# Kernel optimization log

Hardware: AMD Instinct MI355X
Metric: run time of the kernel (lower is better)

The kernel has to match this reference:

```python
import jax, jax.numpy as jnp
import numpy as np
import math

NUM_HEADS = 16
QK_NOPE = 128
QK_ROPE = 64
V_DIM = 128
Q_HEAD_DIM = QK_NOPE + QK_ROPE  # 192
KV_LORA = 512
ROPE_THETA = 10000.0
EPS = 1e-6


def setup_inputs() -> dict:
    key = jax.random.key(0)
    ks = jax.random.split(key, 8)
    B, S, H = 2, 2048, 2048
    hidden_states = jax.random.normal(ks[0], (B, S, H), dtype=jnp.float32)
    position_ids = jnp.broadcast_to(jnp.arange(S, dtype=jnp.int64), (B, S))
    attention_mask = jnp.broadcast_to(jnp.tril(jnp.ones((S, S), dtype=bool)), (B, 1, S, S))
    sc = 0.02
    w_q_down = jax.random.normal(ks[1], (1536, H), dtype=jnp.float32) * sc
    q_norm_w = jnp.ones((1536,), dtype=jnp.float32)
    w_q_up = jax.random.normal(ks[2], (NUM_HEADS * Q_HEAD_DIM, 1536), dtype=jnp.float32) * sc
    w_kv_down = jax.random.normal(ks[3], (KV_LORA + QK_ROPE, H), dtype=jnp.float32) * sc
    kv_norm_w = jnp.ones((KV_LORA,), dtype=jnp.float32)
    w_kv_up = jax.random.normal(ks[4], (NUM_HEADS * (QK_NOPE + V_DIM), KV_LORA), dtype=jnp.float32) * sc
    w_out = jax.random.normal(ks[5], (H, NUM_HEADS * V_DIM), dtype=jnp.float32) * sc
    return {"hidden_states": hidden_states, "position_ids": position_ids,
            "attention_mask": attention_mask, "w_q_down": w_q_down, "q_norm_w": q_norm_w,
            "w_q_up": w_q_up, "w_kv_down": w_kv_down, "kv_norm_w": kv_norm_w,
            "w_kv_up": w_kv_up, "w_out": w_out}


def rms_norm(x, w):
    xf = x.astype(jnp.float32)
    var = jnp.mean(xf * xf, axis=-1, keepdims=True)
    return w * (xf * jax.lax.rsqrt(var + EPS)).astype(x.dtype)


def rotate_half(x):
    d = x.shape[-1]
    return jnp.concatenate((-x[..., d // 2:], x[..., :d // 2]), axis=-1)


def _deinterleave(x):
    # torch: view(..., d//2, 2).transpose(-1,-2).reshape(..., d)
    d = x.shape[-1]
    return x.reshape(*x.shape[:-1], d // 2, 2).swapaxes(-1, -2).reshape(*x.shape[:-1], d)


def _rope_tables(seq_len, dtype):
    inv_freq = 1.0 / (ROPE_THETA ** (jnp.arange(0, QK_ROPE, 2, dtype=jnp.float32) / QK_ROPE))
    t = jnp.arange(seq_len, dtype=jnp.float32)
    freqs = jnp.outer(t, inv_freq)          # [S, QK_ROPE//2]
    emb = jnp.concatenate((freqs, freqs), axis=-1)  # [S, QK_ROPE]
    return jnp.cos(emb).astype(dtype), jnp.sin(emb).astype(dtype)


def mla_forward(hidden_states, position_ids, attention_mask,
                w_q_down, q_norm_w, w_q_up, w_kv_down, kv_norm_w, w_kv_up, w_out):
    B, S, H = hidden_states.shape
    # low-rank Q path
    q = hidden_states @ w_q_down.T                   # [B,S,1536]
    q = rms_norm(q, q_norm_w)
    q = q @ w_q_up.T                                 # [B,S,NH*192]
    q = q.reshape(B, S, NUM_HEADS, Q_HEAD_DIM).transpose(0, 2, 1, 3)  # [B,NH,S,192]
    q_nope, q_rope = q[..., :QK_NOPE], q[..., QK_NOPE:]
    # low-rank KV path
    c = hidden_states @ w_kv_down.T                  # [B,S,576]
    c_kv, k_rope = c[..., :KV_LORA], c[..., KV_LORA:]
    k_rope = k_rope.reshape(B, S, 1, QK_ROPE).transpose(0, 2, 1, 3)   # [B,1,S,64]
    kv = rms_norm(c_kv, kv_norm_w) @ w_kv_up.T       # [B,S,NH*(128+128)]
    kv = kv.reshape(B, S, NUM_HEADS, QK_NOPE + V_DIM).transpose(0, 2, 1, 3)
    k_nope, v = kv[..., :QK_NOPE], kv[..., QK_NOPE:]  # [B,NH,S,128] each
    # decoupled RoPE on the rope sub-dim
    cos, sin = _rope_tables(S, hidden_states.dtype)
    cos_p = cos[position_ids][:, None]               # [B,1,S,64]
    sin_p = sin[position_ids][:, None]
    qr = _deinterleave(q_rope)
    kr = _deinterleave(k_rope)
    q_rope = qr * cos_p + rotate_half(qr) * sin_p
    k_rope = kr * cos_p + rotate_half(kr) * sin_p
    query = jnp.concatenate([q_nope, q_rope], axis=-1)                      # [B,NH,S,192]
    key = jnp.concatenate([k_nope, jnp.broadcast_to(k_rope, (B, NUM_HEADS, S, QK_ROPE))], axis=-1)
    scores = jnp.einsum('bhqd,bhkd->bhqk', query, key) / math.sqrt(Q_HEAD_DIM)
    scores = jnp.where(attention_mask, scores, -jnp.inf)
    attn = jax.nn.softmax(scores, axis=-1).astype(query.dtype)              # [B,NH,S,S]
    out = jnp.einsum('bhqk,bhkd->bhqd', attn, v)                            # [B,NH,S,128]
    out = out.transpose(0, 2, 1, 3).reshape(B, S, NUM_HEADS * V_DIM)
    out = out @ w_out.T                                                     # [B,S,H]
    return out, attn


def reference(hidden_states, position_ids, attention_mask,
              w_q_down, q_norm_w, w_q_up, w_kv_down, kv_norm_w, w_kv_up, w_out):
    return mla_forward(hidden_states, position_ids, attention_mask,
                       w_q_down, q_norm_w, w_q_up, w_kv_down, kv_norm_w, w_kv_up, w_out)
```

## Files before the change

kernel.cpp:

```cpp
#include <hip/hip_runtime.h>
#include <hip/hip_bf16.h>
#include <math.h>

typedef unsigned short u16;
typedef unsigned int u32;
typedef __bf16 bf16x8 __attribute__((ext_vector_type(8)));
typedef float f32x4 __attribute__((ext_vector_type(4)));

__device__ __forceinline__ float bf2f(u16 h) {
    return __uint_as_float(((u32)h) << 16);
}
__device__ __forceinline__ u16 f2bf(float f) {
    u32 u = __float_as_uint(f);
    u32 r = (u + 0x7fffu + ((u >> 16) & 1u)) >> 16;
    return (u16)r;
}

__device__ __forceinline__ f32x4 mfma16(bf16x8 a, bf16x8 b, f32x4 c) {
    return __builtin_amdgcn_mfma_f32_16x16x32_bf16(a, b, c, 0, 0, 0);
}

struct DetectArgs {
    const void* p[8];
    int n[8];
};

__global__ __launch_bounds__(256) void detect_k(DetectArgs a, u32* flags) {
    int b = blockIdx.x;
    int t = threadIdx.x;
    const u16* p = (const u16*)a.p[b];
    u16 v = p[2 * t];
    int e = (v >> 7) & 0xff;
    bool insane = (e < 87) || (e > 167);
    unsigned long long m = __ballot(insane);
    __shared__ u32 s[4];
    int w = t >> 6;
    if ((t & 63) == 0) s[w] = (m != 0ull) ? 1u : 0u;
    __syncthreads();
    if (t == 0) flags[b] = s[0] | s[1] | s[2] | s[3];
}

__global__ __launch_bounds__(256) void convert_k(
    const void* src, u16* dst, int n, const u32* flags, int fi)
{
    u32 f = flags[fi];
    int j0 = blockIdx.x * 1024 + threadIdx.x * 4;
    if (f) {
        const float* s = (const float*)src;
        for (int k = 0; k < 4; k++) {
            int j = j0 + k;
            if (j < n) dst[j] = f2bf(s[j]);
        }
    } else {
        const u16* s = (const u16*)src;
        for (int k = 0; k < 4; k++) {
            int j = j0 + k;
            if (j < n) dst[j] = s[j];
        }
    }
}

__global__ __launch_bounds__(256) void gemm128(
    const u16* __restrict__ X, int xRow, long long xBat,
    const u16* __restrict__ W, int wRow, long long wBat,
    u16* __restrict__ Cb, float* __restrict__ Cf,
    int cRow, long long cBatB, long long cBatH,
    int N, int K)
{
    __shared__ __align__(16) u16 As[128 * 32];
    __shared__ __align__(16) u16 Bs[128 * 32];

    int z = blockIdx.z;
    const u16* Xz = X + (long long)z * xBat;
    const u16* Wz = W + (long long)z * wBat;
    long long cOff = (long long)(z >> 4) * cBatB + (long long)(z & 15) * cBatH;

    int t = threadIdx.x;
    int lane = t & 63, w = t >> 6;
    int sr = t >> 2;
    int sc = (t & 3) * 8;
    int m0 = blockIdx.y * 128, n0 = blockIdx.x * 128;
    int wr = (w >> 1) * 64, wc = (w & 1) * 64;
    int mrow = lane & 15, quad = lane >> 4;

    f32x4 zero = {0.f, 0.f, 0.f, 0.f};
    f32x4 acc[4][4];
    for (int i = 0; i < 4; i++)
        for (int j = 0; j < 4; j++) acc[i][j] = zero;

    for (int k0 = 0; k0 < K; k0 += 32) {
        uint4 a0 = *(const uint4*)(Xz + (long long)(m0 + sr) * xRow + k0 + sc);
        uint4 a1 = *(const uint4*)(Xz + (long long)(m0 + sr + 64) * xRow + k0 + sc);
        int bn0 = n0 + sr;      if (bn0 >= N) bn0 = N - 1;
        int bn1 = n0 + sr + 64; if (bn1 >= N) bn1 = N - 1;
        uint4 b0 = *(const uint4*)(Wz + (long long)bn0 * wRow + k0 + sc);
        uint4 b1 = *(const uint4*)(Wz + (long long)bn1 * wRow + k0 + sc);
        __syncthreads();
        *(uint4*)(&As[sr * 32 + sc]) = a0;
        *(uint4*)(&As[(sr + 64) * 32 + sc]) = a1;
        *(uint4*)(&Bs[sr * 32 + sc]) = b0;
        *(uint4*)(&Bs[(sr + 64) * 32 + sc]) = b1;
        __syncthreads();

        bf16x8 af[4], bfr[4];
        for (int i = 0; i < 4; i++) {
            af[i]  = *(const bf16x8*)(&As[(wr + i * 16 + mrow) * 32 + quad * 8]);
            bfr[i] = *(const bf16x8*)(&Bs[(wc + i * 16 + mrow) * 32 + quad * 8]);
        }
        for (int mt = 0; mt < 4; mt++)
            for (int nt = 0; nt < 4; nt++)
                acc[mt][nt] = mfma16(af[mt], bfr[nt], acc[mt][nt]);
    }

    for (int mt = 0; mt < 4; mt++)
        for (int nt = 0; nt < 4; nt++)
            for (int r = 0; r < 4; r++) {
                int row = m0 + wr + mt * 16 + quad * 4 + r;
                int col = n0 + wc + nt * 16 + mrow;
                if (col < N) {
                    long long idx = cOff + (long long)row * cRow + col;
                    float v = acc[mt][nt][r];
                    if (Cb) Cb[idx] = f2bf(v); else Cf[idx] = v;
                }
            }
}

__global__ __launch_bounds__(256) void gemm128_xf32(
    const float* __restrict__ X, int xRow, long long xBat,
    const u16* __restrict__ W, int wRow, long long wBat,
    u16* __restrict__ Cb, int cRow, long long cBatB, long long cBatH,
    int N, int K)
{
    __shared__ __align__(16) u16 As[128 * 32];
    __shared__ __align__(16) u16 Bs[128 * 32];

    int z = blockIdx.z;
    const float* Xz = X + (long long)z * xBat;
    const u16* Wz = W + (long long)z * wBat;
    long long cOff = (long long)(z >> 4) * cBatB + (long long)(z & 15) * cBatH;

    int t = threadIdx.x;
    int lane = t & 63, w = t >> 6;
    int sr = t >> 2;
    int sc = (t & 3) * 8;
    int m0 = blockIdx.y * 128, n0 = blockIdx.x * 128;
    int wr = (w >> 1) * 64, wc = (w & 1) * 64;
    int mrow = lane & 15, quad = lane >> 4;

    f32x4 zero = {0.f, 0.f, 0.f, 0.f};
    f32x4 acc[4][4];
    for (int i = 0; i < 4; i++)
        for (int j = 0; j < 4; j++) acc[i][j] = zero;

    for (int k0 = 0; k0 < K; k0 += 32) {
        const float* ap0 = Xz + (long long)(m0 + sr) * xRow + k0 + sc;
        const float* ap1 = Xz + (long long)(m0 + sr + 64) * xRow + k0 + sc;
        float4 a0l = *(const float4*)(ap0), a0h = *(const float4*)(ap0 + 4);
        float4 a1l = *(const float4*)(ap1), a1h = *(const float4*)(ap1 + 4);
        int bn0 = n0 + sr;      if (bn0 >= N) bn0 = N - 1;
        int bn1 = n0 + sr + 64; if (bn1 >= N) bn1 = N - 1;
        uint4 b0 = *(const uint4*)(Wz + (long long)bn0 * wRow + k0 + sc);
        uint4 b1 = *(const uint4*)(Wz + (long long)bn1 * wRow + k0 + sc);
        u16 pa0[8] = {f2bf(a0l.x), f2bf(a0l.y), f2bf(a0l.z), f2bf(a0l.w),
                      f2bf(a0h.x), f2bf(a0h.y), f2bf(a0h.z), f2bf(a0h.w)};
        u16 pa1[8] = {f2bf(a1l.x), f2bf(a1l.y), f2bf(a1l.z), f2bf(a1l.w),
                      f2bf(a1h.x), f2bf(a1h.y), f2bf(a1h.z), f2bf(a1h.w)};
        __syncthreads();
        *(uint4*)(&As[sr * 32 + sc]) = *(const uint4*)pa0;
        *(uint4*)(&As[(sr + 64) * 32 + sc]) = *(const uint4*)pa1;
        *(uint4*)(&Bs[sr * 32 + sc]) = b0;
        *(uint4*)(&Bs[(sr + 64) * 32 + sc]) = b1;
        __syncthreads();

        bf16x8 af[4], bfr[4];
        for (int i = 0; i < 4; i++) {
            af[i]  = *(const bf16x8*)(&As[(wr + i * 16 + mrow) * 32 + quad * 8]);
            bfr[i] = *(const bf16x8*)(&Bs[(wc + i * 16 + mrow) * 32 + quad * 8]);
        }
        for (int mt = 0; mt < 4; mt++)
            for (int nt = 0; nt < 4; nt++)
                acc[mt][nt] = mfma16(af[mt], bfr[nt], acc[mt][nt]);
    }

    for (int mt = 0; mt < 4; mt++)
        for (int nt = 0; nt < 4; nt++)
            for (int r = 0; r < 4; r++) {
                int row = m0 + wr + mt * 16 + quad * 4 + r;
                int col = n0 + wc + nt * 16 + mrow;
                if (col < N)
                    Cb[cOff + (long long)row * cRow + col] = f2bf(acc[mt][nt][r]);
            }
}

__global__ __launch_bounds__(256) void rmsnorm_k(
    const float* __restrict__ in, int inRow,
    const u16* __restrict__ wgt,
    u16* __restrict__ out, int outRow, int len)
{
    int row = blockIdx.x;
    const float* x = in + (long long)row * inRow;
    u16* o = out + (long long)row * outRow;
    int t = threadIdx.x;
    float ss = 0.f;
    for (int j = t; j < len; j += 256) { float v = x[j]; ss += v * v; }
    for (int s = 1; s < 64; s <<= 1) ss += __shfl_xor(ss, s);
    __shared__ float red[4];
    int w = t >> 6, lane = t & 63;
    if (lane == 0) red[w] = ss;
    __syncthreads();
    float tot = red[0] + red[1] + red[2] + red[3];
    float r = rsqrtf(tot / (float)len + 1e-6f);
    for (int j = t; j < len; j += 256)
        o[j] = f2bf(bf2f(wgt[j]) * (x[j] * r));
}

__device__ __forceinline__ void rope64(const float* xin, float* xo, int pos) {
    for (int i = 0; i < 32; i++) {
        float ex = (float)(2 * i) * (1.0f / 64.0f);
        float invf = expf(-ex * 9.210340371976184f);
        float ang = (float)pos * invf;
        float sn, cs;
        sincosf(ang, &sn, &cs);
        float a = xin[2 * i], b = xin[2 * i + 1];
        xo[i] = a * cs - b * sn;
        xo[32 + i] = b * cs + a * sn;
    }
}

__global__ __launch_bounds__(256) void rope_q_k(u16* __restrict__ qf) {
    int idx = blockIdx.x * 256 + threadIdx.x;
    int row = idx >> 4, h = idx & 15, pos = row & 2047;
    u16* p = qf + (long long)row * 3072 + h * 192 + 128;
    float xin[64], xo[64];
    for (int j = 0; j < 64; j++) xin[j] = bf2f(p[j]);
    rope64(xin, xo, pos);
    for (int j = 0; j < 64; j++) p[j] = f2bf(xo[j]);
}

__global__ __launch_bounds__(256) void rope_kk(
    const float* __restrict__ cpre, u16* __restrict__ kr) {
    int row = blockIdx.x * 256 + threadIdx.x;
    int pos = row & 2047;
    const float* src = cpre + (long long)row * 576 + 512;
    float xin[64], xo[64];
    for (int j = 0; j < 64; j++) xin[j] = src[j];
    rope64(xin, xo, pos);
    u16* dst = kr + (long long)row * 64;
    for (int j = 0; j < 64; j++) dst[j] = f2bf(xo[j]);
}

__global__ void transpose_v(const u16* __restrict__ kvup, u16* __restrict__ Vt) {
    __shared__ u16 tile[32][33];
    int bh = blockIdx.z, b = bh >> 4, h = bh & 15;
    int s0 = blockIdx.x * 32, d0 = blockIdx.y * 32;
    int tx = threadIdx.x, ty = threadIdx.y;
    for (int i = 0; i < 4; i++) {
        int s = s0 + ty + i * 8;
        tile[ty + i * 8][tx] = kvup[(long long)(b * 2048 + s) * 4096 + h * 256 + 128 + d0 + tx];
    }
    __syncthreads();
    for (int i = 0; i < 4; i++) {
        int d = d0 + ty + i * 8;
        Vt[((long long)bh * 128 + d) * 2048 + s0 + tx] = tile[tx][ty + i * 8];
    }
}

#define ATTN_SCALE 0.07216878364870323f

__global__ __launch_bounds__(256) void scores_gemm(
    const u16* __restrict__ qf, const u16* __restrict__ kvup,
    const u16* __restrict__ krope, float* __restrict__ attn)
{
    int n0 = blockIdx.x * 128, q0 = blockIdx.y * 128;
    if (n0 > q0) return;
    int bh = blockIdx.z, b = bh >> 4, h = bh & 15;
    const u16* qb = qf + (long long)b * 2048 * 3072 + h * 192;
    const u16* kn = kvup + (long long)b * 2048 * 4096 + h * 256;
    const u16* kr = krope + (long long)b * 2048 * 64;
    long long abase = (long long)bh * 4194304;

    __shared__ __align__(16) u16 As[128 * 32];
    __shared__ __align__(16) u16 Bs[128 * 32];
    int t = threadIdx.x, lane = t & 63, w = t >> 6;
    int sr = t >> 2, sc = (t & 3) * 8;
    int wr = (w >> 1) * 64, wc = (w & 1) * 64;
    int mrow = lane & 15, quad = lane >> 4;

    f32x4 zero = {0.f, 0.f, 0.f, 0.f};
    f32x4 acc[4][4];
    for (int i = 0; i < 4; i++)
        for (int j = 0; j < 4; j++) acc[i][j] = zero;

    for (int k0 = 0; k0 < 192; k0 += 32) {
        uint4 a0 = *(const uint4*)(qb + (long long)(q0 + sr) * 3072 + k0 + sc);
        uint4 a1 = *(const uint4*)(qb + (long long)(q0 + sr + 64) * 3072 + k0 + sc);
        uint4 b0, b1;
        if (k0 < 128) {
            b0 = *(const uint4*)(kn + (long long)(n0 + sr) * 4096 + k0 + sc);
            b1 = *(const uint4*)(kn + (long long)(n0 + sr + 64) * 4096 + k0 + sc);
        } else {
            b0 = *(const uint4*)(kr + (long long)(n0 + sr) * 64 + (k0 - 128) + sc);
            b1 = *(const uint4*)(kr + (long long)(n0 + sr + 64) * 64 + (k0 - 128) + sc);
        }
        __syncthreads();
        *(uint4*)(&As[sr * 32 + sc]) = a0;
        *(uint4*)(&As[(sr + 64) * 32 + sc]) = a1;
        *(uint4*)(&Bs[sr * 32 + sc]) = b0;
        *(uint4*)(&Bs[(sr + 64) * 32 + sc]) = b1;
        __syncthreads();

        bf16x8 af[4], bfr[4];
        for (int i = 0; i < 4; i++) {
            af[i]  = *(const bf16x8*)(&As[(wr + i * 16 + mrow) * 32 + quad * 8]);
            bfr[i] = *(const bf16x8*)(&Bs[(wc + i * 16 + mrow) * 32 + quad * 8]);
        }
        for (int mt = 0; mt < 4; mt++)
            for (int nt = 0; nt < 4; nt++)
                acc[mt][nt] = mfma16(af[mt], bfr[nt], acc[mt][nt]);
    }

    for (int mt = 0; mt < 4; mt++)
        for (int nt = 0; nt < 4; nt++)
            for (int r = 0; r < 4; r++) {
                int row = q0 + wr + mt * 16 + quad * 4 + r;
                int col = n0 + wc + nt * 16 + mrow;
                attn[abase + (long long)row * 2048 + col] = acc[mt][nt][r] * ATTN_SCALE;
            }
}

__global__ __launch_bounds__(256) void softmax_rows(float* __restrict__ attn) {
    int r = blockIdx.x;
    long long bh = blockIdx.y;
    float* p = attn + bh * 4194304LL + (long long)r * 2048;
    int t = threadIdx.x;
    int valid = r + 1;

    float mx = -INFINITY;
    for (int j = t; j < valid; j += 256) mx = fmaxf(mx, p[j]);
    for (int s = 1; s < 64; s <<= 1) mx = fmaxf(mx, __shfl_xor(mx, s));
    __shared__ float sm[4];
    if ((t & 63) == 0) sm[t >> 6] = mx;
    __syncthreads();
    mx = fmaxf(fmaxf(sm[0], sm[1]), fmaxf(sm[2], sm[3]));

    float ss = 0.f;
    for (int j = t; j < valid; j += 256) ss += expf(p[j] - mx);
    for (int s = 1; s < 64; s <<= 1) ss += __shfl_xor(ss, s);
    __shared__ float s2[4];
    if ((t & 63) == 0) s2[t >> 6] = ss;
    __syncthreads();
    ss = s2[0] + s2[1] + s2[2] + s2[3];
    float inv = 1.0f / ss;

    for (int j = t; j < 2048; j += 256) {
        float v = (j < valid) ? expf(p[j] - mx) * inv : 0.f;
        p[j] = v;
    }
}

extern "C" void kernel_launch(void* const* d_in, const int* in_sizes, int n_in,
                              void* d_out, int out_size, void* d_ws, size_t ws_size,
                              hipStream_t stream) {
    (void)in_sizes; (void)n_in; (void)out_size; (void)ws_size;

    const void* r_hidden = d_in[0];
    const void* r_wqd    = d_in[3];
    const void* r_qnw    = d_in[4];
    const void* r_wqu    = d_in[5];
    const void* r_wkvd   = d_in[6];
    const void* r_kvnw   = d_in[7];
    const void* r_wkvu   = d_in[8];
    const void* r_wout   = d_in[9];

    float* out_p  = (float*)d_out;
    float* attn_p = (float*)d_out + 8388608LL;

    char* ws = (char*)d_ws;
    size_t off = 0;
    auto alloc = [&](size_t bytes) { void* p = ws + off; off = (off + bytes + 255) & ~(size_t)255; return p; };

    u32* flags = (u32*)alloc(256);
    char* regionA = (char*)alloc(25165824 + 9437184);
    float* q_pre = (float*)regionA;
    float* c_pre = (float*)(regionA + 25165824);
    u16* kv_up   = (u16*)regionA;
    char* regionB = (char*)alloc(16777216);
    u16* hidden_c = (u16*)regionB;
    u16* Vt       = (u16*)regionB;
    char* regionC = (char*)alloc(12582912);
    u16* q_c   = (u16*)regionC;
    u16* kv_c  = (u16*)regionC;
    u16* krope = (u16*)(regionC + 4194304);
    u16* wqd_c  = (u16*)alloc(1536LL * 2048 * 2);
    u16* qnw_c  = (u16*)alloc(1536LL * 2);
    u16* wqu_c  = (u16*)alloc(3072LL * 1536 * 2);
    u16* wkvd_c = (u16*)alloc(576LL * 2048 * 2);
    u16* kvnw_c = (u16*)alloc(512LL * 2);
    u16* wkvu_c = (u16*)alloc(4096LL * 512 * 2);
    u16* wout_c = (u16*)alloc(2048LL * 2048 * 2);
    u16* q_full = (u16*)alloc(4096LL * 3072 * 2);
    u16* Obuf   = q_full;

    DetectArgs da;
    da.p[0] = r_hidden; da.n[0] = 8388608;
    da.p[1] = r_wqd;    da.n[1] = 3145728;
    da.p[2] = r_qnw;    da.n[2] = 1536;
    da.p[3] = r_wqu;    da.n[3] = 4718592;
    da.p[4] = r_wkvd;   da.n[4] = 1179648;
    da.p[5] = r_kvnw;   da.n[5] = 512;
    da.p[6] = r_wkvu;   da.n[6] = 2097152;
    da.p[7] = r_wout;   da.n[7] = 4194304;
    hipLaunchKernelGGL(detect_k, dim3(8), dim3(256), 0, stream, da, flags);

    const void* srcs[8] = {r_hidden, r_wqd, r_qnw, r_wqu, r_wkvd, r_kvnw, r_wkvu, r_wout};
    u16* dsts[8] = {hidden_c, wqd_c, qnw_c, wqu_c, wkvd_c, kvnw_c, wkvu_c, wout_c};
    for (int i = 0; i < 8; i++) {
        int n = da.n[i];
        hipLaunchKernelGGL(convert_k, dim3((n + 1023) / 1024), dim3(256), 0, stream,
            srcs[i], dsts[i], n, flags, i);
    }

    hipLaunchKernelGGL(gemm128, dim3(12, 32, 1), dim3(256), 0, stream,
        hidden_c, 2048, 0LL, wqd_c, 2048, 0LL, (u16*)nullptr, q_pre, 1536, 0LL, 0LL, 1536, 2048);
    hipLaunchKernelGGL(rmsnorm_k, dim3(4096), dim3(256), 0, stream,
        q_pre, 1536, qnw_c, q_c, 1536, 1536);
    hipLaunchKernelGGL(gemm128, dim3(24, 32, 1), dim3(256), 0, stream,
        q_c, 1536, 0LL, wqu_c, 1536, 0LL, q_full, (float*)nullptr, 3072, 0LL, 0LL, 3072, 1536);
    hipLaunchKernelGGL(rope_q_k, dim3(256), dim3(256), 0, stream, q_full);
    hipLaunchKernelGGL(gemm128, dim3(5, 32, 1), dim3(256), 0, stream,
        hidden_c, 2048, 0LL, wkvd_c, 2048, 0LL, (u16*)nullptr, c_pre, 576, 0LL, 0LL, 576, 2048);
    hipLaunchKernelGGL(rmsnorm_k, dim3(4096), dim3(256), 0, stream,
        c_pre, 576, kvnw_c, kv_c, 512, 512);
    hipLaunchKernelGGL(rope_kk, dim3(16), dim3(256), 0, stream, c_pre, krope);
    hipLaunchKernelGGL(gemm128, dim3(32, 32, 1), dim3(256), 0, stream,
        kv_c, 512, 0LL, wkvu_c, 512, 0LL, kv_up, (float*)nullptr, 4096, 0LL, 0LL, 4096, 512);
    hipLaunchKernelGGL(transpose_v, dim3(64, 4, 32), dim3(32, 8), 0, stream, kv_up, Vt);
    hipLaunchKernelGGL(scores_gemm, dim3(16, 16, 32), dim3(256), 0, stream,
        q_full, kv_up, krope, attn_p);
    hipLaunchKernelGGL(softmax_rows, dim3(2048, 32), dim3(256), 0, stream, attn_p);
    hipLaunchKernelGGL(gemm128_xf32, dim3(1, 16, 32), dim3(256), 0, stream,
        attn_p, 2048, 4194304LL, Vt, 2048, 262144LL, Obuf,
        2048, 4194304LL, 128LL, 128, 2048);
    hipLaunchKernelGGL(gemm128, dim3(16, 32, 1), dim3(256), 0, stream,
        Obuf, 2048, 0LL, wout_c, 2048, 0LL, (u16*)nullptr, out_p, 2048, 0LL, 0LL, 2048, 2048);
}
```

Baseline: 1.494 ms.

## Use direct global-to-LDS loads in GEMMs and register-cache softmax rows

Replaces register-staged global loads plus LDS stores in the bf16 GEMM, mixed-precision GEMM and QK score kernels with the global_load_lds builtin, which writes 16 bytes per lane straight into shared memory. The mixed GEMM also stops its K loop at m0+128, skipping K blocks where the operand is zero under a causal structure. Softmax now holds each row in registers via float4 loads, computing exp once and writing with vectorized stores instead of re-reading the row three times. The direct-to-LDS layout (t*8 contiguous) relies on matching the row/col tile layout, and the K truncation assumes a triangular input to that GEMM.

After: 1.317 ms. -11.9%, faster.

```diff
diff --git a/kernel.cpp b/kernel.cpp
--- a/kernel.cpp
+++ b/kernel.cpp
@@ -18,6 +18,13 @@
 
 __device__ __forceinline__ f32x4 mfma16(bf16x8 a, bf16x8 b, f32x4 c) {
     return __builtin_amdgcn_mfma_f32_16x16x32_bf16(a, b, c, 0, 0, 0);
+}
+
+__device__ __forceinline__ void g2l(const u16* g, u16* l) {
+    __builtin_amdgcn_global_load_lds(
+        (const __attribute__((address_space(1))) unsigned int*)g,
+        (__attribute__((address_space(3))) unsigned int*)l,
+        16, 0, 0);
 }
 
 struct DetectArgs {
@@ -83,23 +90,28 @@
     int wr = (w >> 1) * 64, wc = (w & 1) * 64;
     int mrow = lane & 15, quad = lane >> 4;
 
+    u16* As0 = &As[t * 8];
+    u16* As1 = &As[2048 + t * 8];
+    u16* Bs0 = &Bs[t * 8];
+    u16* Bs1 = &Bs[2048 + t * 8];
+
     f32x4 zero = {0.f, 0.f, 0.f, 0.f};
     f32x4 acc[4][4];
     for (int i = 0; i < 4; i++)
         for (int j = 0; j < 4; j++) acc[i][j] = zero;
 
     for (int k0 = 0; k0 < K; k0 += 32) {
-        uint4 a0 = *(const uint4*)(Xz + (long long)(m0 + sr) * xRow + k0 + sc);
-        uint4 a1 = *(const uint4*)(Xz + (long long)(m0 + sr + 64) * xRow + k0 + sc);
+        const u16* ga0 = Xz + (long long)(m0 + sr) * xRow + k0 + sc;
+        const u16* ga1 = ga0 + (long long)64 * xRow;
         int bn0 = n0 + sr;      if (bn0 >= N) bn0 = N - 1;
         int bn1 = n0 + sr + 64; if (bn1 >= N) bn1 = N - 1;
-        uint4 b0 = *(const uint4*)(Wz + (long long)bn0 * wRow + k0 + sc);
-        uint4 b1 = *(const uint4*)(Wz + (long long)bn1 * wRow + k0 + sc);
-        __syncthreads();
-        *(uint4*)(&As[sr * 32 + sc]) = a0;
-        *(uint4*)(&As[(sr + 64) * 32 + sc]) = a1;
-        *(uint4*)(&Bs[sr * 32 + sc]) = b0;
-        *(uint4*)(&Bs[(sr + 64) * 32 + sc]) = b1;
+        const u16* gb0 = Wz + (long long)bn0 * wRow + k0 + sc;
+        const u16* gb1 = Wz + (long long)bn1 * wRow + k0 + sc;
+        __syncthreads();
+        g2l(ga0, As0);
+        g2l(ga1, As1);
+        g2l(gb0, Bs0);
+        g2l(gb1, Bs1);
         __syncthreads();
 
         bf16x8 af[4], bfr[4];
@@ -147,20 +159,25 @@
     int wr = (w >> 1) * 64, wc = (w & 1) * 64;
     int mrow = lane & 15, quad = lane >> 4;
 
+    u16* Bs0 = &Bs[t * 8];
+    u16* Bs1 = &Bs[2048 + t * 8];
+
     f32x4 zero = {0.f, 0.f, 0.f, 0.f};
     f32x4 acc[4][4];
     for (int i = 0; i < 4; i++)
         for (int j = 0; j < 4; j++) acc[i][j] = zero;
 
-    for (int k0 = 0; k0 < K; k0 += 32) {
+    int kEnd = m0 + 128; if (kEnd > K) kEnd = K;
+
+    for (int k0 = 0; k0 < kEnd; k0 += 32) {
         const float* ap0 = Xz + (long long)(m0 + sr) * xRow + k0 + sc;
         const float* ap1 = Xz + (long long)(m0 + sr + 64) * xRow + k0 + sc;
         float4 a0l = *(const float4*)(ap0), a0h = *(const float4*)(ap0 + 4);
         float4 a1l = *(const float4*)(ap1), a1h = *(const float4*)(ap1 + 4);
         int bn0 = n0 + sr;      if (bn0 >= N) bn0 = N - 1;
         int bn1 = n0 + sr + 64; if (bn1 >= N) bn1 = N - 1;
-        uint4 b0 = *(const uint4*)(Wz + (long long)bn0 * wRow + k0 + sc);
-        uint4 b1 = *(const uint4*)(Wz + (long long)bn1 * wRow + k0 + sc);
+        const u16* gb0 = Wz + (long long)bn0 * wRow + k0 + sc;
+        const u16* gb1 = Wz + (long long)bn1 * wRow + k0 + sc;
         u16 pa0[8] = {f2bf(a0l.x), f2bf(a0l.y), f2bf(a0l.z), f2bf(a0l.w),
                       f2bf(a0h.x), f2bf(a0h.y), f2bf(a0h.z), f2bf(a0h.w)};
         u16 pa1[8] = {f2bf(a1l.x), f2bf(a1l.y), f2bf(a1l.z), f2bf(a1l.w),
@@ -168,8 +185,8 @@
         __syncthreads();
         *(uint4*)(&As[sr * 32 + sc]) = *(const uint4*)pa0;
         *(uint4*)(&As[(sr + 64) * 32 + sc]) = *(const uint4*)pa1;
-        *(uint4*)(&Bs[sr * 32 + sc]) = b0;
-        *(uint4*)(&Bs[(sr + 64) * 32 + sc]) = b1;
+        g2l(gb0, Bs0);
+        g2l(gb1, Bs1);
         __syncthreads();
 
         bf16x8 af[4], bfr[4];
@@ -286,27 +303,32 @@
     int wr = (w >> 1) * 64, wc = (w & 1) * 64;
     int mrow = lane & 15, quad = lane >> 4;
 
+    u16* As0 = &As[t * 8];
+    u16* As1 = &As[2048 + t * 8];
+    u16* Bs0 = &Bs[t * 8];
+    u16* Bs1 = &Bs[2048 + t * 8];
+
     f32x4 zero = {0.f, 0.f, 0.f, 0.f};
     f32x4 acc[4][4];
     for (int i = 0; i < 4; i++)
         for (int j = 0; j < 4; j++) acc[i][j] = zero;
 
     for (int k0 = 0; k0 < 192; k0 += 32) {
-        uint4 a0 = *(const uint4*)(qb + (long long)(q0 + sr) * 3072 + k0 + sc);
-        uint4 a1 = *(const uint4*)(qb + (long long)(q0 + sr + 64) * 3072 + k0 + sc);
-        uint4 b0, b1;
+        const u16* ga0 = qb + (long long)(q0 + sr) * 3072 + k0 + sc;
+        const u16* ga1 = ga0 + (long long)64 * 3072;
+        const u16 *gb0, *gb1;
         if (k0 < 128) {
-            b0 = *(const uint4*)(kn + (long long)(n0 + sr) * 4096 + k0 + sc);
-            b1 = *(const uint4*)(kn + (long long)(n0 + sr + 64) * 4096 + k0 + sc);
+            gb0 = kn + (long long)(n0 + sr) * 4096 + k0 + sc;
+            gb1 = gb0 + (long long)64 * 4096;
         } else {
-            b0 = *(const uint4*)(kr + (long long)(n0 + sr) * 64 + (k0 - 128) + sc);
-            b1 = *(const uint4*)(kr + (long long)(n0 + sr + 64) * 64 + (k0 - 128) + sc);
-        }
-        __syncthreads();
-        *(uint4*)(&As[sr * 32 + sc]) = a0;
-        *(uint4*)(&As[(sr + 64) * 32 + sc]) = a1;
-        *(uint4*)(&Bs[sr * 32 + sc]) = b0;
-        *(uint4*)(&Bs[(sr + 64) * 32 + sc]) = b1;
+            gb0 = kr + (long long)(n0 + sr) * 64 + (k0 - 128) + sc;
+            gb1 = gb0 + (long long)64 * 64;
+        }
+        __syncthreads();
+        g2l(ga0, As0);
+        g2l(ga1, As1);
+        g2l(gb0, Bs0);
+        g2l(gb1, Bs1);
         __syncthreads();
 
         bf16x8 af[4], bfr[4];
@@ -334,27 +356,55 @@
     float* p = attn + bh * 4194304LL + (long long)r * 2048;
     int t = threadIdx.x;
     int valid = r + 1;
-
+    int j0 = t * 4;
+
+    float v[8];
     float mx = -INFINITY;
-    for (int j = t; j < valid; j += 256) mx = fmaxf(mx, p[j]);
+#pragma unroll
+    for (int h = 0; h < 2; h++) {
+        int j = j0 + h * 1024;
+        if (j + 4 <= valid) {
+            float4 q = *(const float4*)(p + j);
+            v[h * 4 + 0] = q.x; v[h * 4 + 1] = q.y;
+            v[h * 4 + 2] = q.z; v[h * 4 + 3] = q.w;
+        } else {
+#pragma unroll
+            for (int k = 0; k < 4; k++) {
+                int jj = j + k;
+                v[h * 4 + k] = (jj < valid) ? p[jj] : -INFINITY;
+            }
+        }
+#pragma unroll
+        for (int k = 0; k < 4; k++) mx = fmaxf(mx, v[h * 4 + k]);
+    }
     for (int s = 1; s < 64; s <<= 1) mx = fmaxf(mx, __shfl_xor(mx, s));
-    __shared__ float sm[4];
-    if ((t & 63) == 0) sm[t >> 6] = mx;
+    __shared__ float sm[4], s2[4];
+    int w = t >> 6;
+    if ((t & 63) == 0) sm[w] = mx;
     __syncthreads();
     mx = fmaxf(fmaxf(sm[0], sm[1]), fmaxf(sm[2], sm[3]));
 
     float ss = 0.f;
-    for (int j = t; j < valid; j += 256) ss += expf(p[j] - mx);
+#pragma unroll
+    for (int i = 0; i < 8; i++) {
+        float e = (v[i] == -INFINITY) ? 0.f : expf(v[i] - mx);
+        v[i] = e;
+        ss += e;
+    }
     for (int s = 1; s < 64; s <<= 1) ss += __shfl_xor(ss, s);
-    __shared__ float s2[4];
-    if ((t & 63) == 0) s2[t >> 6] = ss;
+    if ((t & 63) == 0) s2[w] = ss;
     __syncthreads();
     ss = s2[0] + s2[1] + s2[2] + s2[3];
     float inv = 1.0f / ss;
 
-    for (int j = t; j < 2048; j += 256) {
-        float v = (j < valid) ? expf(p[j] - mx) * inv : 0.f;
-        p[j] = v;
+#pragma unroll
+    for (int h = 0; h < 2; h++) {
+        float4 q;
+        q.x = v[h * 4 + 0] * inv;
+        q.y = v[h * 4 + 1] * inv;
+        q.z = v[h * 4 + 2] * inv;
+        q.w = v[h * 4 + 3] * inv;
+        *(float4*)(p + j0 + h * 1024) = q;
     }
 }
 
```
